# Optimization experiments

Hardware: AMD Instinct MI355X
Metric: run time of the kernel (lower is better)

## Reference

```python
import jax, jax.numpy as jnp
import numpy as np

B, DV, DT, H, G, E = 4096, 1024, 1024, 1024, 4096, 8
D = DV + DT  # fused dim = 2048


def setup_inputs() -> dict:
    key = jax.random.key(0)
    ks = jax.random.split(key, 8)
    s = 0.02
    return {
        "vision_cls": jax.random.normal(ks[0], (B, DV), jnp.float32),
        "text_cls": jax.random.normal(ks[1], (B, DT), jnp.float32),
        "W1_imm": jax.random.normal(ks[2], (E, D, H), jnp.float32) * s,
        "b1_imm": jnp.zeros((E, H), jnp.float32),
        "W2_imm": jax.random.normal(ks[3], (E, H, 1), jnp.float32) * s,
        "b2_imm": jnp.zeros((E, 1), jnp.float32),
        "W1_gene": jax.random.normal(ks[4], (E, D, H), jnp.float32) * s,
        "b1_gene": jnp.zeros((E, H), jnp.float32),
        "W2_gene": jax.random.normal(ks[5], (E, H, G), jnp.float32) * s,
        "b2_gene": jnp.zeros((E, G), jnp.float32),
        "organ_idx": jax.random.randint(ks[6], (B,), 0, E, jnp.int32),
    }


def reference(vision_cls, text_cls, W1_imm, b1_imm, W2_imm, b2_imm,
              W1_gene, b1_gene, W2_gene, b2_gene, organ_idx):
    # fused features [B, D]
    fused = jnp.concatenate([vision_cls, text_cls], axis=-1)
    # Dense MoE reference: run every organ head on the full batch, then
    # select each sample's routed output (same math as the per-group
    # gather -> MLP -> scatter in the original; dropout is eval-mode identity).
    h_i = jax.nn.relu(jnp.einsum('bd,edh->ebh', fused, W1_imm) + b1_imm[:, None, :])
    imm_all = jnp.einsum('ebh,eh->eb', h_i, W2_imm[:, :, 0]) + b2_imm[:, :1]  # [E,B]
    h_g = jax.nn.relu(jnp.einsum('bd,edh->ebh', fused, W1_gene) + b1_gene[:, None, :])
    gene_all = jnp.einsum('ebh,ehg->ebg', h_g, W2_gene) + b2_gene[:, None, :]  # [E,B,G]
    bidx = jnp.arange(fused.shape[0])
    immune = imm_all[organ_idx, bidx]      # [B]
    gene = gene_all[organ_idx, bidx]       # [B,G] (uniform gene_dim -> no padding needed)
    return immune, gene, vision_cls, text_cls
```

## Files before the change

### kernel.cpp

```cpp
#include <hip/hip_runtime.h>


#define B_N 4096
#define DV  1024
#define DD  2048
#define HH  1024
#define GG  4096
#define EE  8
#define BM  128
#define MAXRB 40
#define PERM_N (MAXRB * BM)

typedef __bf16 bf16x8 __attribute__((ext_vector_type(8)));
typedef float f32x4 __attribute__((ext_vector_type(4)));
typedef unsigned short u16x4v __attribute__((ext_vector_type(4)));
typedef unsigned short u16x8v __attribute__((ext_vector_type(8)));

#define H_CNT 0
#define H_FIL 8
#define H_OFF 16
#define H_NRB 24
#define H_BLK 32

static __device__ __forceinline__ unsigned short f2bf(float f) {
  return __builtin_bit_cast(unsigned short, (__bf16)f);
}
static __device__ __forceinline__ float bf2f(unsigned short s) {
  return __builtin_bit_cast(float, (unsigned)s << 16);
}
static __device__ __forceinline__ void gload16(const void* g, void* l) {
  __builtin_amdgcn_global_load_lds(
      (const __attribute__((address_space(1))) unsigned int*)g,
      (__attribute__((address_space(3))) unsigned int*)l, 16, 0, 0);
}

__global__ __launch_bounds__(1024) void routing(const int* __restrict__ organ,
                                                int* __restrict__ hdr,
                                                int* __restrict__ perm) {
  __shared__ int cnt[EE], fil[EE], off[EE];
  const int tid = threadIdx.x;
  if (tid < EE) { cnt[tid] = 0; fil[tid] = 0; }
  __syncthreads();
#pragma unroll
  for (int i = 0; i < 4; ++i) atomicAdd(&cnt[organ[tid + (i << 10)]], 1);
#pragma unroll
  for (int i = 0; i < 5; ++i) perm[tid + (i << 10)] = -1;
  __syncthreads();
  if (tid == 0) {
    int acc = 0;
    for (int e = 0; e < EE; ++e) {
      off[e] = acc;
      hdr[H_OFF + e] = acc;
      hdr[H_CNT + e] = cnt[e];
      int nb = (cnt[e] + BM - 1) >> 7;
      int rb0 = acc >> 7;
      for (int i = 0; i < nb; ++i) hdr[H_BLK + rb0 + i] = e;
      acc += nb << 7;
    }
    hdr[H_NRB] = acc >> 7;
  }
  __syncthreads();
#pragma unroll
  for (int i = 0; i < 4; ++i) {
    int b = tid + (i << 10);
    int e = organ[b];
    int slot = off[e] + atomicAdd(&fil[e], 1);
    perm[slot] = b;
  }
}

__global__ __launch_bounds__(256) void k_A(
    const float* __restrict__ vis, const float* __restrict__ txt,
    const int* __restrict__ hdr, const int* __restrict__ perm,
    unsigned short* __restrict__ Abuf) {
  const int bx = blockIdx.x;
  const int nr = hdr[H_NRB] << 7;
  const int tid = threadIdx.x;
  const int c = tid << 3;
  const float* srcbase = (c < DV) ? vis : txt;
  const int cc = (c < DV) ? c : c - DV;
#pragma unroll
  for (int p = 0; p < 4; ++p) {
    int r = (bx << 2) + p;
    if (r >= nr) return;
    int smp = perm[r];
    u16x8v v;
    if (smp >= 0) {
      const float* src = srcbase + (size_t)smp * 1024 + cc;
      float4 a = *(const float4*)src, b = *(const float4*)(src + 4);
      v[0] = f2bf(a.x); v[1] = f2bf(a.y); v[2] = f2bf(a.z); v[3] = f2bf(a.w);
      v[4] = f2bf(b.x); v[5] = f2bf(b.y); v[6] = f2bf(b.z); v[7] = f2bf(b.w);
    } else {
#pragma unroll
      for (int i = 0; i < 8; ++i) v[i] = 0;
    }
    *(u16x8v*)&Abuf[(size_t)r * DD + c] = v;
  }
}

static __device__ __forceinline__ void copy_body(
    int bx, const float4* __restrict__ v, const float4* __restrict__ t,
    float4* __restrict__ ov, float4* __restrict__ ot) {
  const int n4 = B_N * DV / 4;
  for (int i = bx * 256 + (int)threadIdx.x; i < n4; i += 1024 * 256) {
    ov[i] = v[i];
    ot[i] = t[i];
  }
}

template <int KDIM, int NST>
static __device__ __forceinline__ void gemm_core(
    const unsigned short* __restrict__ Aseg,
    const float* __restrict__ Bglob,
    unsigned short* smem, f32x4 (&acc)[4][4]) {
  const int tid = threadIdx.x;
  const int lane = tid & 63;
  const int wr = ((tid >> 6) >> 1) << 6, wc = ((tid >> 6) & 1) << 6;
  const int lr = lane & 15;
  const int arow = tid >> 2;
  const int kq_src = (((tid & 3) ^ ((arow >> 1) & 3)) << 3);
  const int wbase = (tid & 192) << 3;
  const int bn4 = (tid & 31) << 2;
  const int bk4 = (tid >> 5) << 2;
  constexpr int NT = KDIM / 32;

  float4 bvA[4], bvB[4];

  auto issueA = [&](int buf, int k0) {
    gload16(Aseg + (size_t)arow * KDIM + k0 + kq_src, smem + (buf << 12) + wbase);
    gload16(Aseg + (size_t)(64 + arow) * KDIM + k0 + kq_src,
            smem + (buf << 12) + 2048 + wbase);
  };
  auto issueB = [&](float4 (&bv)[4], int k0) {
    const float* p = Bglob + (size_t)(k0 + bk4) * NST + bn4;
#pragma unroll
    for (int i = 0; i < 4; ++i) bv[i] = *(const float4*)(p + (size_t)i * NST);
  };
  auto writeB = [&](int buf, float4 (&bv)[4]) {
    const float* f0 = (const float*)&bv[0];
    const float* f1 = (const float*)&bv[1];
    const float* f2 = (const float*)&bv[2];
    const float* f3 = (const float*)&bv[3];
#pragma unroll
    for (int j = 0; j < 4; ++j) {
      const int n = bn4 + j;
      const int s3 = (n ^ (n >> 3)) & 7;
      u16x4v w;
      w[0] = f2bf(f0[j]); w[1] = f2bf(f1[j]);
      w[2] = f2bf(f2[j]); w[3] = f2bf(f3[j]);
      *(u16x4v*)(smem + 8192 + (buf << 12) + (n << 5) + ((((bk4 >> 2)) ^ s3) << 2)) = w;
    }
  };
  auto compute = [&](int buf) {
    bf16x8 af[4], bfr[4];
#pragma unroll
    for (int m = 0; m < 4; ++m) {
      const int r = wr + m * 16 + lr;
      const int cs = ((lane >> 4) ^ ((r >> 1) & 3)) << 3;
      af[m] = *(const bf16x8*)&smem[(buf << 12) + r * 32 + cs];
    }
#pragma unroll
    for (int n = 0; n < 4; ++n) {
      const int fr = wc + n * 16 + lr;
      const int s3 = (fr ^ (fr >> 3)) & 7;
      const unsigned short* row = smem + 8192 + (buf << 12) + (fr << 5);
      const int g = (lane >> 4) << 1;
      union { unsigned long long q[2]; bf16x8 v; } u;
      u.q[0] = *(const unsigned long long*)(row + ((g ^ s3) << 2));
      u.q[1] = *(const unsigned long long*)(row + (((g + 1) ^ s3) << 2));
      bfr[n] = u.v;
    }
#pragma unroll
    for (int m = 0; m < 4; ++m)
#pragma unroll
      for (int n = 0; n < 4; ++n)
        acc[m][n] = __builtin_amdgcn_mfma_f32_16x16x32_bf16(af[m], bfr[n], acc[m][n], 0, 0, 0);
  };

  issueB(bvA, 0);
  writeB(0, bvA);
  issueA(0, 0);
  __builtin_amdgcn_sched_barrier(0);
  issueB(bvB, 1 << 5);
  asm volatile("s_waitcnt vmcnt(4) lgkmcnt(0)" ::: "memory");
  __builtin_amdgcn_s_barrier();

  int t = 0;
  for (; t + 2 < NT; t += 2) {
    issueA(1, (t + 1) << 5);
    __builtin_amdgcn_sched_barrier(0);
    issueB(bvA, (t + 2) << 5);
    compute(0);
    writeB(1, bvB);
    asm volatile("s_waitcnt vmcnt(4) lgkmcnt(0)" ::: "memory");
    __builtin_amdgcn_s_barrier();
    issueA(0, (t + 2) << 5);
    __builtin_amdgcn_sched_barrier(0);
    issueB(bvB, (t + 3) << 5);
    compute(1);
    writeB(0, bvA);
    asm volatile("s_waitcnt vmcnt(4) lgkmcnt(0)" ::: "memory");
    __builtin_amdgcn_s_barrier();
  }
  issueA(1, (NT - 1) << 5);
  compute(0);
  writeB(1, bvB);
  asm volatile("s_waitcnt vmcnt(0) lgkmcnt(0)" ::: "memory");
  __builtin_amdgcn_s_barrier();
  compute(1);
}

#define G_L1 (MAXRB * 16)
__global__ __launch_bounds__(256) void k_L1(
    const unsigned short* __restrict__ Abuf, const float* __restrict__ W1i,
    const float* __restrict__ W1g, const float* __restrict__ b1i,
    const float* __restrict__ b1g, const int* __restrict__ hdr,
    unsigned short* __restrict__ H1, unsigned short* __restrict__ H2,
    const float4* __restrict__ vis4, const float4* __restrict__ txt4,
    float4* __restrict__ ov, float4* __restrict__ ot) {
  __shared__ __align__(16) unsigned short smem[16384];
  int bx = blockIdx.x;
  if (bx >= G_L1) { copy_body(bx - G_L1, vis4, txt4, ov, ot); return; }
  const int id = (bx & 7) * (G_L1 >> 3) + (bx >> 3);
  const int rb = id % MAXRB;
  if (rb >= hdr[H_NRB]) return;
  const int sub = id / MAXRB, head = sub >> 3, cb = (sub & 7) << 7;
  const int e = hdr[H_BLK + rb];
  const float* Bglob = (head ? W1g : W1i) + (size_t)e * DD * HH + cb;
  const float* bias = (head ? b1g : b1i) + e * HH;
  unsigned short* Hout = head ? H2 : H1;
  const int tid = threadIdx.x;
  const int lane = tid & 63, wave = tid >> 6;
  const int wr = (wave >> 1) << 6, wc = (wave & 1) << 6;
  const int lr = lane & 15;

  f32x4 acc[4][4];
#pragma unroll
  for (int m = 0; m < 4; ++m)
#pragma unroll
    for (int n = 0; n < 4; ++n) acc[m][n] = (f32x4){0.f, 0.f, 0.f, 0.f};

  gemm_core<DD, HH>(Abuf + (size_t)rb * BM * DD, Bglob, smem, acc);
  __syncthreads();

  const int r0l = wr + ((lane >> 4) << 2);
#pragma unroll
  for (int n = 0; n < 4; ++n) {
    const int col = wc + n * 16 + lr;
    const float bv = bias[cb + col];
#pragma unroll
    for (int m = 0; m < 4; ++m)
#pragma unroll
      for (int v = 0; v < 4; ++v) {
        int row = r0l + m * 16 + v;
        float x = acc[m][n][v] + bv;
        x = x > 0.f ? x : 0.f;
        smem[((row << 7) + col) ^ ((row & 7) << 3)] = f2bf(x);
      }
  }
  __syncthreads();
#pragma unroll
  for (int c = 0; c < 8; ++c) {
    int q = c * 256 + tid;
    int row = q >> 4, ch = q & 15;
    int off = ((row << 7) + (ch << 3)) ^ ((row & 7) << 3);
    u16x8v val = *(const u16x8v*)&smem[off];
    *(u16x8v*)&Hout[(size_t)(rb * BM + row) * HH + cb + (ch << 3)] = val;
  }
}

static __device__ __forceinline__ void immune_body(
    int bx, const int* __restrict__ hdr, const int* __restrict__ perm,
    const unsigned short* __restrict__ H1, const float* __restrict__ W2,
    const float* __restrict__ b2, float* __restrict__ out) {
  const int nrb = hdr[H_NRB];
  const int r = bx * 4 + (threadIdx.x >> 6);
  if (r >= nrb * BM) return;
  const int b = perm[r];
  if (b < 0) return;
  const int e = hdr[H_BLK + (r >> 7)];
  const int lane = threadIdx.x & 63;
  const unsigned short* h = H1 + (size_t)r * HH + lane * 16;
  const float* w = W2 + (size_t)e * HH + lane * 16;
  float s = 0.f;
#pragma unroll
  for (int i = 0; i < 16; ++i) s += bf2f(h[i]) * w[i];
#pragma unroll
  for (int off = 32; off >= 1; off >>= 1) s += __shfl_xor(s, off, 64);
  if (lane == 0) out[b] = s + b2[e];
}

#define G_L2 (MAXRB * 32)
__global__ __launch_bounds__(256) void k_L2(
    const unsigned short* __restrict__ H2buf, const float* __restrict__ W2g,
    const float* __restrict__ b2g, const int* __restrict__ hdr,
    const int* __restrict__ perm, float* __restrict__ outg,
    const unsigned short* __restrict__ H1, const float* __restrict__ W2i,
    const float* __restrict__ b2i, float* __restrict__ outi) {
  __shared__ __align__(16) unsigned short smem[16384];
  int bx = blockIdx.x;
  if (bx >= G_L2) {
    immune_body(bx - G_L2, hdr, perm, H1, W2i, b2i, outi);
    return;
  }
  const int id = (bx & 7) * (G_L2 >> 3) + (bx >> 3);
  const int rb = id % MAXRB;
  if (rb >= hdr[H_NRB]) return;
  const int cb = (id / MAXRB) << 7;
  const int e = hdr[H_BLK + rb];
  const float* Bglob = W2g + (size_t)e * HH * GG + cb;
  const int tid = threadIdx.x;
  const int lane = tid & 63, wave = tid >> 6;
  const int wr = (wave >> 1) << 6, wc = (wave & 1) << 6;
  const int lr = lane & 15;

  f32x4 acc[4][4];
#pragma unroll
  for (int m = 0; m < 4; ++m)
#pragma unroll
    for (int n = 0; n < 4; ++n) acc[m][n] = (f32x4){0.f, 0.f, 0.f, 0.f};

  gemm_core<HH, GG>(H2buf + (size_t)rb * BM * HH, Bglob, smem, acc);
  __syncthreads();

  const int r0l = wr + ((lane >> 4) << 2);
#pragma unroll
  for (int n = 0; n < 4; ++n) {
    const int col = wc + n * 16 + lr;
    const float bv = b2g[e * GG + cb + col];
#pragma unroll
    for (int m = 0; m < 4; ++m)
#pragma unroll
      for (int v = 0; v < 4; ++v) {
        int row = r0l + m * 16 + v;
        smem[((row << 7) + col) ^ ((row & 7) << 3)] = f2bf(acc[m][n][v] + bv);
      }
  }
  __syncthreads();
#pragma unroll
  for (int c = 0; c < 8; ++c) {
    int q = c * 256 + tid;
    int row = q >> 4, ch = q & 15;
    int sm = perm[rb * BM + row];
    if (sm < 0) continue;
    int off = ((row << 7) + (ch << 3)) ^ ((row & 7) << 3);
    u16x8v val = *(const u16x8v*)&smem[off];
    float4 f0, f1;
    f0.x = bf2f(val[0]); f0.y = bf2f(val[1]); f0.z = bf2f(val[2]); f0.w = bf2f(val[3]);
    f1.x = bf2f(val[4]); f1.y = bf2f(val[5]); f1.z = bf2f(val[6]); f1.w = bf2f(val[7]);
    float* dst = outg + (size_t)sm * GG + cb + (ch << 3);
    *(float4*)dst = f0;
    *(float4*)(dst + 4) = f1;
  }
}

extern "C" void kernel_launch(void* const* d_in, const int* in_sizes, int n_in,
                              void* d_out, int out_size, void* d_ws, size_t ws_size,
                              hipStream_t stream) {
  (void)in_sizes; (void)n_in; (void)out_size; (void)ws_size;
  const float* vis = (const float*)d_in[0];
  const float* txt = (const float*)d_in[1];
  const float* W1i = (const float*)d_in[2];
  const float* b1i = (const float*)d_in[3];
  const float* W2i = (const float*)d_in[4];
  const float* b2i = (const float*)d_in[5];
  const float* W1g = (const float*)d_in[6];
  const float* b1g = (const float*)d_in[7];
  const float* W2g = (const float*)d_in[8];
  const float* b2g = (const float*)d_in[9];
  const int* organ = (const int*)d_in[10];

  float* out_imm = (float*)d_out;
  float* out_gene = out_imm + B_N;
  float* out_vis = out_gene + (size_t)B_N * GG;
  float* out_txt = out_vis + (size_t)B_N * DV;

  int* hdr = (int*)d_ws;
  int* perm = hdr + 128;

  const size_t OFF_ABUF = 32768;
  const size_t OFF_H1 = OFF_ABUF + (size_t)PERM_N * DD * 2;
  const size_t OFF_H2 = OFF_H1 + (size_t)PERM_N * HH * 2;
  unsigned short* Abuf = (unsigned short*)((char*)d_ws + OFF_ABUF);
  unsigned short* H1 = (unsigned short*)((char*)d_ws + OFF_H1);
  unsigned short* H2 = (unsigned short*)((char*)d_ws + OFF_H2);

  routing<<<1, 1024, 0, stream>>>(organ, hdr, perm);
  k_A<<<PERM_N / 4, 256, 0, stream>>>(vis, txt, hdr, perm, Abuf);
  k_L1<<<G_L1 + 1024, 256, 0, stream>>>(Abuf, W1i, W1g, b1i, b1g, hdr, H1, H2,
                                        (const float4*)vis, (const float4*)txt,
                                        (float4*)out_vis, (float4*)out_txt);
  k_L2<<<G_L2 + PERM_N / 4, 256, 0, stream>>>(H2, W2g, b2g, hdr, perm, out_gene,
                                              H1, W2i, b2i, out_imm);
}
```

Before: 259.0 us.

## Deepen A-tile prefetch to four LDS buffers with a distance-three pipeline

The GEMM core now rotates the A tile through four LDS buffers, so A loads are issued three k-steps ahead instead of one. The B tile stays double-buffered through registers. The explicit vmcnt waits are dropped; ordering relies on waits the compiler inserts before the B register data is used. The aim is to hide global load latency better, at the cost of more LDS per block (24576 instead of 16384 unsigned shorts), which may cut the number of resident blocks per CU.

```diff
diff --git a/kernel.cpp b/kernel.cpp
--- a/kernel.cpp
+++ b/kernel.cpp
@@ -124,12 +124,12 @@
   const int bk4 = (tid >> 5) << 2;
   constexpr int NT = KDIM / 32;
 
-  float4 bvA[4], bvB[4];
+  float4 bvE[4], bvO[4];
 
   auto issueA = [&](int buf, int k0) {
-    gload16(Aseg + (size_t)arow * KDIM + k0 + kq_src, smem + (buf << 12) + wbase);
-    gload16(Aseg + (size_t)(64 + arow) * KDIM + k0 + kq_src,
-            smem + (buf << 12) + 2048 + wbase);
+    unsigned short* d = smem + (buf << 12) + wbase;
+    gload16(Aseg + (size_t)arow * KDIM + k0 + kq_src, d);
+    gload16(Aseg + (size_t)(64 + arow) * KDIM + k0 + kq_src, d + 2048);
   };
   auto issueB = [&](float4 (&bv)[4], int k0) {
     const float* p = Bglob + (size_t)(k0 + bk4) * NST + bn4;
@@ -148,22 +148,22 @@
       u16x4v w;
       w[0] = f2bf(f0[j]); w[1] = f2bf(f1[j]);
       w[2] = f2bf(f2[j]); w[3] = f2bf(f3[j]);
-      *(u16x4v*)(smem + 8192 + (buf << 12) + (n << 5) + ((((bk4 >> 2)) ^ s3) << 2)) = w;
-    }
-  };
-  auto compute = [&](int buf) {
+      *(u16x4v*)(smem + 16384 + (buf << 12) + (n << 5) + ((((bk4 >> 2)) ^ s3) << 2)) = w;
+    }
+  };
+  auto compute = [&](int ab, int bb) {
     bf16x8 af[4], bfr[4];
 #pragma unroll
     for (int m = 0; m < 4; ++m) {
       const int r = wr + m * 16 + lr;
       const int cs = ((lane >> 4) ^ ((r >> 1) & 3)) << 3;
-      af[m] = *(const bf16x8*)&smem[(buf << 12) + r * 32 + cs];
+      af[m] = *(const bf16x8*)&smem[(ab << 12) + r * 32 + cs];
     }
 #pragma unroll
     for (int n = 0; n < 4; ++n) {
       const int fr = wc + n * 16 + lr;
       const int s3 = (fr ^ (fr >> 3)) & 7;
-      const unsigned short* row = smem + 8192 + (buf << 12) + (fr << 5);
+      const unsigned short* row = smem + 16384 + (bb << 12) + (fr << 5);
       const int g = (lane >> 4) << 1;
       union { unsigned long long q[2]; bf16x8 v; } u;
       u.q[0] = *(const unsigned long long*)(row + ((g ^ s3) << 2));
@@ -177,37 +177,35 @@
         acc[m][n] = __builtin_amdgcn_mfma_f32_16x16x32_bf16(af[m], bfr[n], acc[m][n], 0, 0, 0);
   };
 
-  issueB(bvA, 0);
-  writeB(0, bvA);
+  auto phase = [&](int t, float4 (&bvIss)[4], float4 (&bvWr)[4]) {
+    if (t + 3 < NT) issueA((t + 3) & 3, (t + 3) << 5);
+    __builtin_amdgcn_sched_barrier(0);
+    if (t + 2 < NT) issueB(bvIss, (t + 2) << 5);
+    __builtin_amdgcn_sched_barrier(0);
+    compute(t & 3, t & 1);
+    if (t + 1 < NT) writeB((t + 1) & 1, bvWr);
+    asm volatile("s_waitcnt lgkmcnt(0)" ::: "memory");
+    __builtin_amdgcn_s_barrier();
+    __builtin_amdgcn_sched_barrier(0);
+  };
+
   issueA(0, 0);
   __builtin_amdgcn_sched_barrier(0);
-  issueB(bvB, 1 << 5);
-  asm volatile("s_waitcnt vmcnt(4) lgkmcnt(0)" ::: "memory");
+  issueB(bvE, 0);
+  writeB(0, bvE);
+  issueA(1, 1 << 5);
+  __builtin_amdgcn_sched_barrier(0);
+  issueA(2, 2 << 5);
+  __builtin_amdgcn_sched_barrier(0);
+  issueB(bvO, 1 << 5);
+  asm volatile("s_waitcnt lgkmcnt(0)" ::: "memory");
   __builtin_amdgcn_s_barrier();
-
-  int t = 0;
-  for (; t + 2 < NT; t += 2) {
-    issueA(1, (t + 1) << 5);
-    __builtin_amdgcn_sched_barrier(0);
-    issueB(bvA, (t + 2) << 5);
-    compute(0);
-    writeB(1, bvB);
-    asm volatile("s_waitcnt vmcnt(4) lgkmcnt(0)" ::: "memory");
-    __builtin_amdgcn_s_barrier();
-    issueA(0, (t + 2) << 5);
-    __builtin_amdgcn_sched_barrier(0);
-    issueB(bvB, (t + 3) << 5);
-    compute(1);
-    writeB(0, bvA);
-    asm volatile("s_waitcnt vmcnt(4) lgkmcnt(0)" ::: "memory");
-    __builtin_amdgcn_s_barrier();
-  }
-  issueA(1, (NT - 1) << 5);
-  compute(0);
-  writeB(1, bvB);
-  asm volatile("s_waitcnt vmcnt(0) lgkmcnt(0)" ::: "memory");
-  __builtin_amdgcn_s_barrier();
-  compute(1);
+  __builtin_amdgcn_sched_barrier(0);
+
+  for (int t = 0; t < NT; t += 2) {
+    phase(t, bvE, bvO);
+    phase(t + 1, bvO, bvE);
+  }
 }
 
 #define G_L1 (MAXRB * 16)
@@ -218,7 +216,7 @@
     unsigned short* __restrict__ H1, unsigned short* __restrict__ H2,
     const float4* __restrict__ vis4, const float4* __restrict__ txt4,
     float4* __restrict__ ov, float4* __restrict__ ot) {
-  __shared__ __align__(16) unsigned short smem[16384];
+  __shared__ __align__(16) unsigned short smem[24576];
   int bx = blockIdx.x;
   if (bx >= G_L1) { copy_body(bx - G_L1, vis4, txt4, ov, ot); return; }
   const int id = (bx & 7) * (G_L1 >> 3) + (bx >> 3);
@@ -297,7 +295,7 @@
     const int* __restrict__ perm, float* __restrict__ outg,
     const unsigned short* __restrict__ H1, const float* __restrict__ W2i,
     const float* __restrict__ b2i, float* __restrict__ outi) {
-  __shared__ __align__(16) unsigned short smem[16384];
+  __shared__ __align__(16) unsigned short smem[24576];
   int bx = blockIdx.x;
   if (bx >= G_L2) {
     immune_body(bx - G_L2, hdr, perm, H1, W2i, b2i, outi);
```

After: 250.3 us. -3.4%, faster.
